# Kernel tuning notes

Measured on AMD Instinct MI355X. Metric: run time of the kernel, lower is better.

Reference implementation:

```python
import jax, jax.numpy as jnp
import numpy as np

V_CHUNK = 2048  # module default v_chunk


def _chunked_ce(h, W, labels, weights, v_chunk):
    """Weighted mean CE computed with a flash-style online logsumexp over
    vocab chunks, never materializing the full [N, V] logits tensor."""
    N, D = h.shape
    V = W.shape[0]
    n_chunks = V // v_chunk
    Wc = W.reshape(n_chunks, v_chunk, D)          # [C, vc, D]
    offs = jnp.arange(n_chunks) * v_chunk          # chunk start indices
    rows = jnp.arange(N)

    def body(carry, xs):
        m, s, lab = carry                          # running max, sum(exp), label logit
        Wk, off = xs
        logits = h @ Wk.T                          # [N, vc] chunk logits
        cmax = logits.max(axis=1)
        m_new = jnp.maximum(m, cmax)
        s = s * jnp.exp(m - m_new) + jnp.exp(logits - m_new[:, None]).sum(axis=1)
        idx = labels - off
        in_chunk = (idx >= 0) & (idx < v_chunk)
        gathered = logits[rows, jnp.clip(idx, 0, v_chunk - 1)]
        lab = lab + jnp.where(in_chunk, gathered, jnp.float32(0))
        return (m_new, s, lab), None

    init = (jnp.full((N,), -jnp.inf, dtype=h.dtype),
            jnp.zeros((N,), dtype=h.dtype),
            jnp.zeros((N,), dtype=h.dtype))
    # checkpoint the body so chunk logits are recomputed, not stored
    (m, s, lab), _ = jax.lax.scan(jax.checkpoint(body), init, (Wc, offs))
    lse = m + jnp.log(s)                           # [N]
    nll = lse - lab                                # [N] per-token NLL
    return jnp.sum(weights * nll) / jnp.sum(weights)


def setup_inputs() -> dict:
    key = jax.random.key(0)
    k1, k2, k3, k4 = jax.random.split(key, 4)
    B, S, D, V = 1, 4096, 2048, 65536
    h = jax.random.normal(k1, (B, S, D), dtype=jnp.float32)
    W = jax.random.normal(k2, (V, D), dtype=jnp.float32) * 0.02
    labels = jax.random.randint(k3, (B, S), 0, V, dtype=jnp.int64)
    loss_weights = jax.random.uniform(k4, (B, S), dtype=jnp.float32)
    return {"hidden_states": h, "labels": labels,
            "loss_weights": loss_weights, "W": W}


def reference(hidden_states, labels, loss_weights, W):
    D = hidden_states.shape[-1]
    h_flat = hidden_states.reshape(-1, D)
    labels_flat = labels.reshape(-1)
    weights_flat = loss_weights.reshape(-1)
    return _chunked_ce(h_flat, W, labels_flat, weights_flat, V_CHUNK)
```

## Files before the change

### kernel.cpp

```cpp
#include <hip/hip_runtime.h>


typedef __attribute__((ext_vector_type(4)))  float f32x4;
typedef __attribute__((ext_vector_type(8)))  float f32x8;
typedef __attribute__((ext_vector_type(4)))  int   i32x4;

#define N_TOK 4096
#define DIM   2048
#define VOCAB 65536
#define BM    128
#define BN    256
#define BK    64
#define NT    (DIM / BK)
#define NCH   (VOCAB / BN)
#define NTB   (N_TOK / BM)

__device__ __forceinline__ void gload_lds16(const void* g, void* l) {
    __builtin_amdgcn_global_load_lds(
        (const __attribute__((address_space(1))) void*)g,
        (__attribute__((address_space(3))) void*)l, 16, 0, 0);
}

__device__ __forceinline__ void bar() {
    asm volatile("" ::: "memory");
    __builtin_amdgcn_s_barrier();
    asm volatile("" ::: "memory");
}

__global__ __launch_bounds__(256) void convert_f32_i8(
    const float* __restrict__ src, signed char* __restrict__ dst,
    long n, float scale)
{
    long i = ((long)blockIdx.x * 256 + threadIdx.x) * 8;
    if (i + 8 > n) return;
    f32x8 v = *(const f32x8*)(src + i);
    signed char o[8];
    #pragma unroll
    for (int j = 0; j < 8; ++j) {
        float x = v[j] * scale;
        x = fminf(fmaxf(x, -127.0f), 127.0f);
        o[j] = (signed char)__float2int_rn(x);
    }
    *(uint2*)(dst + i) = *(const uint2*)o;
}

__global__ __launch_bounds__(512, 4) void gemm_lse(
    const signed char* __restrict__ h8,
    const signed char* __restrict__ W8,
    float* __restrict__ part_m, float* __restrict__ part_s, int chunk0)
{
    __shared__ unsigned char A_lds[2][8192];
    __shared__ unsigned char B_lds[2][16384];

    const int tid  = threadIdx.x;
    const int lane = tid & 63;
    const int w    = tid >> 6;
    const int wmr  = w >> 2;
    const int wnc  = w & 3;

    const int nwg  = gridDim.x;
    const int orig = blockIdx.x;
    const int q8 = nwg >> 3, r8 = nwg & 7;
    const int xcd = orig & 7;
    const int wg  = (xcd < r8 ? xcd * (q8 + 1) : r8 * (q8 + 1) + (xcd - r8) * q8)
                    + (orig >> 3);
    const int tok_blk = wg & (NTB - 1);
    const int voc_blk = wg >> 5;

    const long arow0 = (long)tok_blk * BM;
    const signed char* Ab = h8 + arow0 * DIM;
    const signed char* Bb = W8 + (long)voc_blk * BN * DIM;

    i32x4 acc[4][4];
    #pragma unroll
    for (int i = 0; i < 4; ++i)
        #pragma unroll
        for (int j = 0; j < 4; ++j)
            acc[i][j] = (i32x4){0, 0, 0, 0};

    const long soff = (long)(tid >> 2) * DIM + ((tid & 3) ^ ((tid >> 2) & 3)) * 16;
    const int  sdb  = w * 1024;

#define SW_A(t, PD)                                                           \
    gload_lds16(Ab + (t) * BK + soff, (char*)&A_lds[PD][0] + sdb);
#define SW_B(t, PD, j)                                                        \
    gload_lds16(Bb + (t) * BK + soff + (long)(j) * 128 * DIM,                 \
                (char*)&B_lds[PD][0] + sdb + (j) * 8192);

    const int rbase = (lane & 15) * 64 + (((lane >> 4) ^ (lane & 3)) * 16);

#define KTILE(CUR, NXT, t)                                                    \
    {                                                                         \
        if ((t) + 1 < NT) {                                                   \
            SW_A((t) + 1, NXT)                                                \
            SW_B((t) + 1, NXT, 0)                                             \
            SW_B((t) + 1, NXT, 1)                                             \
        }                                                                     \
        const char* Ah = (const char*)&A_lds[CUR][0] + wmr * 4096 + rbase;    \
        const char* Bh = (const char*)&B_lds[CUR][0] + wnc * 4096 + rbase;    \
        i32x4 aR[4], bR[4];                                                   \
        _Pragma("unroll")                                                     \
        for (int m = 0; m < 4; ++m) aR[m] = *(const i32x4*)(Ah + m * 1024);   \
        _Pragma("unroll")                                                     \
        for (int n = 0; n < 4; ++n) bR[n] = *(const i32x4*)(Bh + n * 1024);   \
        __builtin_amdgcn_s_setprio(1);                                        \
        _Pragma("unroll")                                                     \
        for (int m = 0; m < 4; ++m)                                           \
            _Pragma("unroll")                                                 \
            for (int n = 0; n < 4; ++n)                                       \
                acc[m][n] = __builtin_amdgcn_mfma_i32_16x16x64_i8(            \
                    aR[m], bR[n], acc[m][n], 0, 0, 0);                        \
        __builtin_amdgcn_s_setprio(0);                                        \
        asm volatile("s_waitcnt vmcnt(0)" ::: "memory");                      \
        bar();                                                                \
    }

    SW_A(0, 0) SW_B(0, 0, 0) SW_B(0, 0, 1)
    asm volatile("s_waitcnt vmcnt(0)" ::: "memory");
    bar();

    for (int t = 0; t < NT; t += 2) {
        KTILE(0, 1, t)
        KTILE(1, 0, t + 1)
    }
#undef KTILE
#undef SW_A
#undef SW_B

    const float INV = 1.0f / 16384.0f;
    float* red_m = (float*)&A_lds[0][0];
    float* red_s = ((float*)&A_lds[0][0]) + 512;
    #pragma unroll
    for (int m = 0; m < 4; ++m) {
        #pragma unroll
        for (int r = 0; r < 4; ++r) {
            float v0 = (float)acc[m][0][r] * INV;
            float v1 = (float)acc[m][1][r] * INV;
            float v2 = (float)acc[m][2][r] * INV;
            float v3 = (float)acc[m][3][r] * INV;
            float mx = fmaxf(fmaxf(v0, v1), fmaxf(v2, v3));
            #pragma unroll
            for (int msk = 1; msk < 16; msk <<= 1)
                mx = fmaxf(mx, __shfl_xor(mx, msk, 64));
            float se = __expf(v0 - mx) + __expf(v1 - mx) +
                       __expf(v2 - mx) + __expf(v3 - mx);
            #pragma unroll
            for (int msk = 1; msk < 16; msk <<= 1)
                se += __shfl_xor(se, msk, 64);
            if ((lane & 15) == 0) {
                const int row = wmr * 64 + m * 16 + (lane >> 4) * 4 + r;
                red_m[row * 4 + wnc] = mx;
                red_s[row * 4 + wnc] = se;
            }
        }
    }
    __syncthreads();
    if (tid < BM) {
        float M = red_m[tid * 4], S = red_s[tid * 4];
        #pragma unroll
        for (int j = 1; j < 4; ++j) {
            const float m2 = red_m[tid * 4 + j], s2 = red_s[tid * 4 + j];
            const float Mn = fmaxf(M, m2);
            S = S * __expf(M - Mn) + s2 * __expf(m2 - Mn);
            M = Mn;
        }
        part_m[(arow0 + tid) * NCH + chunk0 + voc_blk] = M;
        part_s[(arow0 + tid) * NCH + chunk0 + voc_blk] = S;
    }
}

__global__ __launch_bounds__(256) void label_dot(
    const float* __restrict__ h, const float* __restrict__ W,
    const void* __restrict__ labels, float* __restrict__ lab_logit)
{
    bool is64 = true;
    #pragma unroll
    for (int i = 0; i < 8; ++i) {
        long long v = ((const long long*)labels)[i];
        if (v < 0 || v >= VOCAB) is64 = false;
    }
    const int t = blockIdx.x;
    const int lab = is64 ? (int)((const long long*)labels)[t]
                         : ((const int*)labels)[t];
    const float4* hp = (const float4*)(h + (long)t * DIM);
    const float4* wp = (const float4*)(W + (long)lab * DIM);
    float s = 0.f;
    #pragma unroll
    for (int j = 0; j < 2; ++j) {
        const float4 a = hp[threadIdx.x + j * 256];
        const float4 b = wp[threadIdx.x + j * 256];
        s += a.x * b.x + a.y * b.y + a.z * b.z + a.w * b.w;
    }
    #pragma unroll
    for (int msk = 1; msk < 64; msk <<= 1) s += __shfl_xor(s, msk, 64);
    __shared__ float ps[4];
    if ((threadIdx.x & 63) == 0) ps[threadIdx.x >> 6] = s;
    __syncthreads();
    if (threadIdx.x == 0) lab_logit[t] = ps[0] + ps[1] + ps[2] + ps[3];
}

__global__ __launch_bounds__(256) void finalize_nll(
    const float* __restrict__ part_m, const float* __restrict__ part_s,
    const float* __restrict__ lab_logit, const float* __restrict__ wts,
    float* __restrict__ wnll)
{
    const int t    = blockIdx.x * 4 + (threadIdx.x >> 6);
    const int lane = threadIdx.x & 63;
    float m = -3.4e38f, s = 0.f;
    #pragma unroll
    for (int j = 0; j < 4; ++j) {
        const int c = j * 64 + lane;
        const float pm = part_m[(long)t * NCH + c];
        const float ps = part_s[(long)t * NCH + c];
        const float M = fmaxf(m, pm);
        s = s * __expf(m - M) + ps * __expf(pm - M);
        m = M;
    }
    #pragma unroll
    for (int msk = 1; msk < 64; msk <<= 1) {
        const float om = __shfl_xor(m, msk, 64);
        const float os = __shfl_xor(s, msk, 64);
        const float M = fmaxf(m, om);
        s = s * __expf(m - M) + os * __expf(om - M);
        m = M;
    }
    if (lane == 0) {
        const float lse = m + logf(s);
        wnll[t] = wts[t] * (lse - lab_logit[t]);
    }
}

__global__ __launch_bounds__(1024) void final_reduce(
    const float* __restrict__ wnll, const float* __restrict__ wts,
    float* __restrict__ out)
{
    float a = 0.f, b = 0.f;
    #pragma unroll
    for (int j = 0; j < 4; ++j) {
        const int i = threadIdx.x + j * 1024;
        a += wnll[i];
        b += wts[i];
    }
    #pragma unroll
    for (int msk = 1; msk < 64; msk <<= 1) {
        a += __shfl_xor(a, msk, 64);
        b += __shfl_xor(b, msk, 64);
    }
    __shared__ float pa[16], pb[16];
    if ((threadIdx.x & 63) == 0) {
        pa[threadIdx.x >> 6] = a;
        pb[threadIdx.x >> 6] = b;
    }
    __syncthreads();
    if (threadIdx.x == 0) {
        float A = 0.f, B = 0.f;
        #pragma unroll
        for (int i = 0; i < 16; ++i) { A += pa[i]; B += pb[i]; }
        out[0] = A / B;
    }
}

extern "C" void kernel_launch(void* const* d_in, const int* in_sizes, int n_in,
                              void* d_out, int out_size, void* d_ws, size_t ws_size,
                              hipStream_t stream)
{
    const float* h      = (const float*)d_in[0];
    const void*  labels = d_in[1];
    const float* wts    = (const float*)d_in[2];
    const float* W      = (const float*)d_in[3];
    float* out = (float*)d_out;

    char* ws = (char*)d_ws;
    signed char*    h8        = (signed char*)(ws);
    float*          part_m    = (float*)(ws + (16u << 20));
    float*          part_s    = (float*)(ws + (24u << 20));
    float*          lab_logit = (float*)(ws + (32u << 20));
    float*          wnll      = (float*)(ws + (32u << 20) + 16384);
    signed char*    wseg      = (signed char*)(ws + (32u << 20) + 32768);
    const size_t base = (size_t)(32u << 20) + 32768;

    long segmax = 0;
    if (ws_size > base) segmax = (long)((ws_size - base) / (size_t)DIM);
    segmax &= ~255L;
    if (segmax > VOCAB) segmax = VOCAB;
    if (segmax < 256)   segmax = 256;

    convert_f32_i8<<<(N_TOK * DIM) / (256 * 8), 256, 0, stream>>>(
        h, h8, (long)N_TOK * DIM, 16.0f);

    for (long v0 = 0; v0 < VOCAB; v0 += segmax) {
        const long rows = (VOCAB - v0) < segmax ? (VOCAB - v0) : segmax;
        convert_f32_i8<<<(int)(rows * DIM / (256 * 8)), 256, 0, stream>>>(
            W + v0 * DIM, wseg, rows * (long)DIM, 1024.0f);
        const int nwg = (int)(rows / BN) * NTB;
        gemm_lse<<<nwg, 512, 0, stream>>>(h8, wseg, part_m, part_s,
                                          (int)(v0 / BN));
    }

    label_dot<<<N_TOK, 256, 0, stream>>>(h, W, labels, lab_logit);

    finalize_nll<<<N_TOK / 4, 256, 0, stream>>>(part_m, part_s, lab_logit,
                                                wts, wnll);

    final_reduce<<<1, 1024, 0, stream>>>(wnll, wts, out);
}
```

Baseline: 798.3 us.

## Enlarge GEMM token tile to 256 rows with 8x4 MFMA per wave

Doubles the token block from 128 to 256 rows, so each wave computes an 8x4 grid of 16x16 int8 MFMA tiles and the A LDS buffer doubles. Each loaded W tile is reused across twice as many tokens, which halves the redundant W reads and raises MFMA work per LDS load. In exchange, accumulator registers double and launch bounds drop to 2 blocks per CU, which lowers occupancy and latency hiding. The grid now has half as many workgroups.

```diff
diff --git a/kernel.cpp b/kernel.cpp
--- a/kernel.cpp
+++ b/kernel.cpp
@@ -8,7 +8,7 @@
 #define N_TOK 4096
 #define DIM   2048
 #define VOCAB 65536
-#define BM    128
+#define BM    256
 #define BN    256
 #define BK    64
 #define NT    (DIM / BK)
@@ -44,19 +44,19 @@
     *(uint2*)(dst + i) = *(const uint2*)o;
 }
 
-__global__ __launch_bounds__(512, 4) void gemm_lse(
+__global__ __launch_bounds__(512, 2) void gemm_lse(
     const signed char* __restrict__ h8,
     const signed char* __restrict__ W8,
     float* __restrict__ part_m, float* __restrict__ part_s, int chunk0)
 {
-    __shared__ unsigned char A_lds[2][8192];
+    __shared__ unsigned char A_lds[2][16384];
     __shared__ unsigned char B_lds[2][16384];
 
     const int tid  = threadIdx.x;
     const int lane = tid & 63;
     const int w    = tid >> 6;
-    const int wmr  = w >> 2;
-    const int wnc  = w & 3;
+    const int wm   = w >> 2;
+    const int wn   = w & 3;
 
     const int nwg  = gridDim.x;
     const int orig = blockIdx.x;
@@ -65,15 +65,15 @@
     const int wg  = (xcd < r8 ? xcd * (q8 + 1) : r8 * (q8 + 1) + (xcd - r8) * q8)
                     + (orig >> 3);
     const int tok_blk = wg & (NTB - 1);
-    const int voc_blk = wg >> 5;
+    const int voc_blk = wg >> 4;
 
     const long arow0 = (long)tok_blk * BM;
     const signed char* Ab = h8 + arow0 * DIM;
     const signed char* Bb = W8 + (long)voc_blk * BN * DIM;
 
-    i32x4 acc[4][4];
-    #pragma unroll
-    for (int i = 0; i < 4; ++i)
+    i32x4 acc[8][4];
+    #pragma unroll
+    for (int i = 0; i < 8; ++i)
         #pragma unroll
         for (int j = 0; j < 4; ++j)
             acc[i][j] = (i32x4){0, 0, 0, 0};
@@ -81,8 +81,9 @@
     const long soff = (long)(tid >> 2) * DIM + ((tid & 3) ^ ((tid >> 2) & 3)) * 16;
     const int  sdb  = w * 1024;
 
-#define SW_A(t, PD)                                                           \
-    gload_lds16(Ab + (t) * BK + soff, (char*)&A_lds[PD][0] + sdb);
+#define SW_A(t, PD, j)                                                        \
+    gload_lds16(Ab + (t) * BK + soff + (long)(j) * 128 * DIM,                 \
+                (char*)&A_lds[PD][0] + sdb + (j) * 8192);
 #define SW_B(t, PD, j)                                                        \
     gload_lds16(Bb + (t) * BK + soff + (long)(j) * 128 * DIM,                 \
                 (char*)&B_lds[PD][0] + sdb + (j) * 8192);
@@ -92,20 +93,19 @@
 #define KTILE(CUR, NXT, t)                                                    \
     {                                                                         \
         if ((t) + 1 < NT) {                                                   \
-            SW_A((t) + 1, NXT)                                                \
-            SW_B((t) + 1, NXT, 0)                                             \
-            SW_B((t) + 1, NXT, 1)                                             \
+            SW_A((t) + 1, NXT, 0) SW_A((t) + 1, NXT, 1)                       \
+            SW_B((t) + 1, NXT, 0) SW_B((t) + 1, NXT, 1)                       \
         }                                                                     \
-        const char* Ah = (const char*)&A_lds[CUR][0] + wmr * 4096 + rbase;    \
-        const char* Bh = (const char*)&B_lds[CUR][0] + wnc * 4096 + rbase;    \
-        i32x4 aR[4], bR[4];                                                   \
-        _Pragma("unroll")                                                     \
-        for (int m = 0; m < 4; ++m) aR[m] = *(const i32x4*)(Ah + m * 1024);   \
+        const char* Ah = (const char*)&A_lds[CUR][0] + wm * 8192 + rbase;     \
+        const char* Bh = (const char*)&B_lds[CUR][0] + wn * 4096 + rbase;     \
+        i32x4 aR[8], bR[4];                                                   \
         _Pragma("unroll")                                                     \
         for (int n = 0; n < 4; ++n) bR[n] = *(const i32x4*)(Bh + n * 1024);   \
+        _Pragma("unroll")                                                     \
+        for (int m = 0; m < 8; ++m) aR[m] = *(const i32x4*)(Ah + m * 1024);   \
         __builtin_amdgcn_s_setprio(1);                                        \
         _Pragma("unroll")                                                     \
-        for (int m = 0; m < 4; ++m)                                           \
+        for (int m = 0; m < 8; ++m)                                           \
             _Pragma("unroll")                                                 \
             for (int n = 0; n < 4; ++n)                                       \
                 acc[m][n] = __builtin_amdgcn_mfma_i32_16x16x64_i8(            \
@@ -115,7 +115,7 @@
         bar();                                                                \
     }
 
-    SW_A(0, 0) SW_B(0, 0, 0) SW_B(0, 0, 1)
+    SW_A(0, 0, 0) SW_A(0, 0, 1) SW_B(0, 0, 0) SW_B(0, 0, 1)
     asm volatile("s_waitcnt vmcnt(0)" ::: "memory");
     bar();
 
@@ -129,15 +129,15 @@
 
     const float INV = 1.0f / 16384.0f;
     float* red_m = (float*)&A_lds[0][0];
-    float* red_s = ((float*)&A_lds[0][0]) + 512;
-    #pragma unroll
-    for (int m = 0; m < 4; ++m) {
+    float* red_s = ((float*)&A_lds[0][0]) + 1024;
+    #pragma unroll
+    for (int mf = 0; mf < 8; ++mf) {
         #pragma unroll
         for (int r = 0; r < 4; ++r) {
-            float v0 = (float)acc[m][0][r] * INV;
-            float v1 = (float)acc[m][1][r] * INV;
-            float v2 = (float)acc[m][2][r] * INV;
-            float v3 = (float)acc[m][3][r] * INV;
+            float v0 = (float)acc[mf][0][r] * INV;
+            float v1 = (float)acc[mf][1][r] * INV;
+            float v2 = (float)acc[mf][2][r] * INV;
+            float v3 = (float)acc[mf][3][r] * INV;
             float mx = fmaxf(fmaxf(v0, v1), fmaxf(v2, v3));
             #pragma unroll
             for (int msk = 1; msk < 16; msk <<= 1)
@@ -148,14 +148,14 @@
             for (int msk = 1; msk < 16; msk <<= 1)
                 se += __shfl_xor(se, msk, 64);
             if ((lane & 15) == 0) {
-                const int row = wmr * 64 + m * 16 + (lane >> 4) * 4 + r;
-                red_m[row * 4 + wnc] = mx;
-                red_s[row * 4 + wnc] = se;
+                const int row = wm * 128 + mf * 16 + (lane >> 4) * 4 + r;
+                red_m[row * 4 + wn] = mx;
+                red_s[row * 4 + wn] = se;
             }
         }
     }
     __syncthreads();
-    if (tid < BM) {
+    if (tid < 256) {
         float M = red_m[tid * 4], S = red_s[tid * 4];
         #pragma unroll
         for (int j = 1; j < 4; ++j) {
```

Measured after the change: 895.6 us. +12.2%, slower.
